# Performance work log

Measured on AMD Instinct MI355X. Metric: run time of the kernel, lower is better.

The kernel has to match this reference:

```python
import jax, jax.numpy as jnp
import numpy as np

TOPK = 8
EXTRA = 0  # ADDITIONAL_LAYERS_IN_GPU
CPU_TOPK = int(0.25 * 64)  # CPU_MOE_RATIO * num_experts = 16


def setup_inputs() -> dict:
    key = jax.random.key(0)
    k1, k2 = jax.random.split(key)
    hidden_states = jax.random.normal(k1, (4, 4096, 4096), dtype=jnp.float32)
    wg_weight = jax.random.normal(k2, (64, 4096), dtype=jnp.float32) * 0.02
    return {"hidden_states": hidden_states, "wg_weight": wg_weight}


def reference(hidden_states, wg_weight):
    bsz, seq_len, hidden_size = hidden_states.shape
    x = hidden_states.reshape(-1, hidden_size).astype(jnp.float32)  # [T, H]
    logits = jnp.einsum('th,eh->te', x, wg_weight)  # [T, 64]
    gates = jax.nn.softmax(logits, axis=1)
    values_all, indices_all = jax.lax.top_k(gates, TOPK + EXTRA)
    expert_weight = values_all[:, :TOPK]
    expert_index = indices_all[:, :TOPK]
    _, cpu_expert_index = jax.lax.top_k(gates, CPU_TOPK)
    cpu_expert_index = cpu_expert_index[:, 8 + EXTRA:]
    # norm_topk_prob=True, topk > 1
    eps = jnp.finfo(jnp.float32).eps
    denom = jnp.maximum(expert_weight.sum(axis=1, keepdims=True), eps)
    expert_weight = expert_weight / denom
    return (expert_weight, expert_index, cpu_expert_index, indices_all)
```

## Files before the change

### kernel.cpp

```cpp
#include <hip/hip_runtime.h>

#define T_TOK 16384
#define HDIM  4096
#define NEXP  64
#define TAU   2e-4f
#define BM    128

typedef unsigned short u16;
typedef u16   u16x8  __attribute__((ext_vector_type(8)));
typedef __bf16 bf16x8 __attribute__((ext_vector_type(8)));
typedef float f32x4  __attribute__((ext_vector_type(4)));

__global__ void zero_counter(int* counter) {
    if (threadIdx.x == 0) counter[0] = 0;
}

__global__ __launch_bounds__(256)
void wsplit_kernel(const float* __restrict__ w, u16x8* __restrict__ wfrag,
                   float4* __restrict__ wt4) {
    const int id  = blockIdx.x * 256 + threadIdx.x;
    const int e   = id >> 9;
    const int k8g = id & 511;
    const int k   = k8g * 8;

    const float* wp = w + (size_t)e * HDIM + k;
    const float4 v0 = *(const float4*)wp;
    const float4 v1 = *(const float4*)(wp + 4);

    wt4[(size_t)(2 * k8g) * NEXP + e]     = v0;
    wt4[(size_t)(2 * k8g + 1) * NEXP + e] = v1;

    const float fv[8] = {v0.x, v0.y, v0.z, v0.w, v1.x, v1.y, v1.z, v1.w};
    bf16x8 hv, lv;
#pragma unroll
    for (int j = 0; j < 8; ++j) {
        const __bf16 h = (__bf16)fv[j];
        hv[j] = h;
        lv[j] = (__bf16)(fv[j] - (float)h);
    }
    const int chunk = k >> 6;
    const int k8 = (k >> 3) & 7, ks = k8 >> 2, g = k8 & 3, nt = e >> 4;
    const int U = ks * 256 + nt * 64 + 16 * g + (e & 15);
    wfrag[(size_t)chunk * 1024 + U]       = __builtin_bit_cast(u16x8, hv);
    wfrag[(size_t)chunk * 1024 + 512 + U] = __builtin_bit_cast(u16x8, lv);
}

__global__ __launch_bounds__(256, 4)
void gate_gemm_mfma(const float* __restrict__ x, const u16x8* __restrict__ wfrag,
                    float* __restrict__ partial, int ksplit) {
    const int b      = blockIdx.x;
    const int kslice = b % ksplit;
    const int tblk   = b / ksplit;
    const int kspan  = HDIM / ksplit;
    const int k0     = kslice * kspan;
    const int t0     = tblk * BM;

    __shared__ __align__(16) u16 smem[2048 * 8];
    u16x8* smemv = (u16x8*)smem;

    const int tid  = threadIdx.x;
    const int lane = tid & 63;
    const int wv   = tid >> 6;

    f32x4 acc[2][4];
#pragma unroll
    for (int m = 0; m < 2; ++m)
#pragma unroll
        for (int nt = 0; nt < 4; ++nt) acc[m][nt] = (f32x4){0.f, 0.f, 0.f, 0.f};

    for (int kc = k0; kc < k0 + kspan; kc += 64) {
        __syncthreads();

#pragma unroll
        for (int i = 0; i < 4; ++i) {
            const int L   = tid + 256 * i;
            const int row = L >> 3;
            const int k8  = L & 7;
            const float* xp = x + (size_t)(t0 + row) * HDIM + kc + 8 * k8;
            const float4 v0 = *(const float4*)xp;
            const float4 v1 = *(const float4*)(xp + 4);
            const float fv[8] = {v0.x, v0.y, v0.z, v0.w, v1.x, v1.y, v1.z, v1.w};
            bf16x8 hv, lv;
#pragma unroll
            for (int j = 0; j < 8; ++j) {
                const __bf16 h = (__bf16)fv[j];
                hv[j] = h;
                lv[j] = (__bf16)(fv[j] - (float)h);
            }
            const int g = k8 & 3, ks = k8 >> 2, mt = row >> 4;
            const int U = ks * 512 + mt * 64 + 16 * g + (row & 15);
            const int phys = U ^ k8;
            smemv[phys]        = __builtin_bit_cast(u16x8, hv);
            smemv[1024 + phys] = __builtin_bit_cast(u16x8, lv);
        }
        __syncthreads();

        const u16x8* wsrc = wfrag + (size_t)(kc >> 6) * 1024;
#pragma unroll
        for (int ks2 = 0; ks2 < 2; ++ks2) {
            const int xo = (ks2 << 2) + (lane >> 4);
            bf16x8 axh[2], axl[2];
#pragma unroll
            for (int m = 0; m < 2; ++m) {
                const int ux = (ks2 * 512 + (wv * 2 + m) * 64 + lane) ^ xo;
                axh[m] = __builtin_bit_cast(bf16x8, smemv[ux]);
                axl[m] = __builtin_bit_cast(bf16x8, smemv[1024 + ux]);
            }
#pragma unroll
            for (int nt = 0; nt < 4; ++nt) {
                const int uwi = ks2 * 256 + nt * 64 + lane;
                const bf16x8 bh = __builtin_bit_cast(bf16x8, wsrc[uwi]);
                const bf16x8 bl = __builtin_bit_cast(bf16x8, wsrc[512 + uwi]);
#pragma unroll
                for (int m = 0; m < 2; ++m) {
                    acc[m][nt] = __builtin_amdgcn_mfma_f32_16x16x32_bf16(axh[m], bh, acc[m][nt], 0, 0, 0);
                    acc[m][nt] = __builtin_amdgcn_mfma_f32_16x16x32_bf16(axh[m], bl, acc[m][nt], 0, 0, 0);
                    acc[m][nt] = __builtin_amdgcn_mfma_f32_16x16x32_bf16(axl[m], bh, acc[m][nt], 0, 0, 0);
                }
            }
        }
    }

    float* op = partial + (size_t)kslice * T_TOK * NEXP;
    const int ecol = lane & 15;
#pragma unroll
    for (int m = 0; m < 2; ++m) {
        const int trow = t0 + (wv * 2 + m) * 16 + ((lane >> 4) << 2);
#pragma unroll
        for (int nt = 0; nt < 4; ++nt)
#pragma unroll
            for (int r = 0; r < 4; ++r)
                op[(size_t)(trow + r) * NEXP + nt * 16 + ecol] = acc[m][nt][r];
    }
}

__global__ __launch_bounds__(256)
void gate_topk_f32(const float* __restrict__ partial, int ksplit,
                   float* __restrict__ out, int* __restrict__ list,
                   int* __restrict__ counter) {
    const int wave = threadIdx.x >> 6;
    const int lane = threadIdx.x & 63;
    const int t = blockIdx.x * 4 + wave;

    float l = 0.f;
    for (int s = 0; s < ksplit; ++s)
        l += partial[(size_t)s * T_TOK * NEXP + (size_t)t * NEXP + lane];

    float v = l;
    const int idx = lane;
    float myval = -3.4e38f;
    int   myidx = 0;
#pragma unroll
    for (int r = 0; r < 17; ++r) {
        float bv = v;
        int   bi = idx;
#pragma unroll
        for (int s = 1; s < 64; s <<= 1) {
            const float ov = __shfl_xor(bv, s);
            const int   oi = __shfl_xor(bi, s);
            if (ov > bv || (ov == bv && oi < bi)) { bv = ov; bi = oi; }
        }
        if (lane == r) { myval = bv; myidx = bi; }
        if (idx == bi) v = -3.4e38f;
    }

    const float nxt = __shfl(myval, (lane + 1) & 63);
    const bool close = (lane < 16) && (myval - nxt < TAU);
    if (__ballot(close) != 0ull) {
        if (lane == 0) { const int p = atomicAdd(counter, 1); list[p] = t; }
    }

    const float m = __shfl(myval, 0);
    const float p = (lane < 16) ? expf(myval - m) : 0.f;
    float s8 = (lane < 8) ? p : 0.f;
#pragma unroll
    for (int s = 1; s < 64; s <<= 1) s8 += __shfl_xor(s8, s);

    float* ew = out;
    float* ei = out + (size_t)T_TOK * 8;
    float* ci = out + (size_t)2 * T_TOK * 8;
    float* ia = out + (size_t)3 * T_TOK * 8;
    if (lane < 8) {
        ew[(size_t)t * 8 + lane] = p / s8;
        ei[(size_t)t * 8 + lane] = (float)myidx;
        ia[(size_t)t * 8 + lane] = (float)myidx;
    } else if (lane < 16) {
        ci[(size_t)t * 8 + (lane - 8)] = (float)myidx;
    }
}

__global__ __launch_bounds__(256)
void repair_partial(const float* __restrict__ x, const float4* __restrict__ wt4,
                    const int* __restrict__ list, const int* __restrict__ counter,
                    double* __restrict__ fpart) {
    const int lane = threadIdx.x & 63;
    const int wid  = (int)((blockIdx.x * blockDim.x + threadIdx.x) >> 6);
    const int nw   = (int)((gridDim.x * blockDim.x) >> 6);
    const int nit  = counter[0] * 16;

    for (int it = wid; it < nit; it += nw) {
        const int li = it >> 4;
        const int ks = it & 15;
        const int t  = __builtin_amdgcn_readfirstlane(list[li]);
        const float4* xr4 = (const float4*)(x + (size_t)t * HDIM) + ks * 64;
        const float4* wb  = wt4 + (size_t)ks * 64 * NEXP;

        double a0 = 0.0, a1 = 0.0, a2 = 0.0, a3 = 0.0;
#pragma unroll 4
        for (int j = 0; j < 64; j += 4) {
            const float4 w0 = wb[(size_t)(j + 0) * NEXP + lane];
            const float4 w1 = wb[(size_t)(j + 1) * NEXP + lane];
            const float4 w2 = wb[(size_t)(j + 2) * NEXP + lane];
            const float4 w3 = wb[(size_t)(j + 3) * NEXP + lane];
            const float4 x0 = xr4[j + 0];
            const float4 x1 = xr4[j + 1];
            const float4 x2 = xr4[j + 2];
            const float4 x3 = xr4[j + 3];
            a0 = fma((double)x0.x, (double)w0.x, a0);
            a0 = fma((double)x0.y, (double)w0.y, a0);
            a0 = fma((double)x0.z, (double)w0.z, a0);
            a0 = fma((double)x0.w, (double)w0.w, a0);
            a1 = fma((double)x1.x, (double)w1.x, a1);
            a1 = fma((double)x1.y, (double)w1.y, a1);
            a1 = fma((double)x1.z, (double)w1.z, a1);
            a1 = fma((double)x1.w, (double)w1.w, a1);
            a2 = fma((double)x2.x, (double)w2.x, a2);
            a2 = fma((double)x2.y, (double)w2.y, a2);
            a2 = fma((double)x2.z, (double)w2.z, a2);
            a2 = fma((double)x2.w, (double)w2.w, a2);
            a3 = fma((double)x3.x, (double)w3.x, a3);
            a3 = fma((double)x3.y, (double)w3.y, a3);
            a3 = fma((double)x3.z, (double)w3.z, a3);
            a3 = fma((double)x3.w, (double)w3.w, a3);
        }
        fpart[(size_t)li * 1024 + ks * 64 + lane] = (a0 + a1) + (a2 + a3);
    }
}

__global__ __launch_bounds__(256)
void repair_final(const double* __restrict__ fpart, const int* __restrict__ list,
                  const int* __restrict__ counter, float* __restrict__ out) {
    const int lane = threadIdx.x & 63;
    const int wid  = (int)((blockIdx.x * blockDim.x + threadIdx.x) >> 6);
    const int nw   = (int)((gridDim.x * blockDim.x) >> 6);
    const int n    = counter[0];

    for (int li = wid; li < n; li += nw) {
        const int t = __builtin_amdgcn_readfirstlane(list[li]);

        double v = 0.0;
#pragma unroll
        for (int ks = 0; ks < 16; ++ks)
            v += fpart[(size_t)li * 1024 + ks * 64 + lane];

        const int idx = lane;
        double mylog = -1.0e308;
        int    myidx = 0;
#pragma unroll
        for (int r = 0; r < 16; ++r) {
            double bv = v;
            int    bi = idx;
#pragma unroll
            for (int s = 1; s < 64; s <<= 1) {
                const double ov = __shfl_xor(bv, s);
                const int    oi = __shfl_xor(bi, s);
                if (ov > bv || (ov == bv && oi < bi)) { bv = ov; bi = oi; }
            }
            if (lane == r) { mylog = bv; myidx = bi; }
            if (idx == bi) v = -1.0e308;
        }

        const double m = __shfl(mylog, 0);
        const float p = (lane < 16) ? expf((float)(mylog - m)) : 0.f;
        float s8 = (lane < 8) ? p : 0.f;
#pragma unroll
        for (int s = 1; s < 64; s <<= 1) s8 += __shfl_xor(s8, s);

        float* ew = out;
        float* ei = out + (size_t)T_TOK * 8;
        float* ci = out + (size_t)2 * T_TOK * 8;
        float* ia = out + (size_t)3 * T_TOK * 8;
        if (lane < 8) {
            ew[(size_t)t * 8 + lane] = p / s8;
            ei[(size_t)t * 8 + lane] = (float)myidx;
            ia[(size_t)t * 8 + lane] = (float)myidx;
        } else if (lane < 16) {
            ci[(size_t)t * 8 + (lane - 8)] = (float)myidx;
        }
    }
}

extern "C" void kernel_launch(void* const* d_in, const int* in_sizes, int n_in,
                              void* d_out, int out_size, void* d_ws, size_t ws_size,
                              hipStream_t stream) {
    const float* x = (const float*)d_in[0];
    const float* w = (const float*)d_in[1];
    float* out     = (float*)d_out;

    const size_t slice      = (size_t)T_TOK * NEXP * sizeof(float);
    const size_t wfragBytes = (size_t)64 * 1024 * 16;
    const size_t wt4Bytes   = (size_t)NEXP * HDIM * sizeof(float);
    const size_t fpartBytes = (size_t)T_TOK * 16 * NEXP * sizeof(double);
    const size_t extra      = wfragBytes + wt4Bytes + fpartBytes +
                              (size_t)T_TOK * sizeof(int) + 64;

    int ksplit = 1;
    if      (ws_size >= 4 * slice + extra) ksplit = 4;
    else if (ws_size >= 2 * slice + extra) ksplit = 2;

    float*  partial = (float*)d_ws;
    u16x8*  wfrag   = (u16x8*)((char*)d_ws + (size_t)ksplit * slice);
    float4* wt4     = (float4*)((char*)wfrag + wfragBytes);
    double* fpart   = (double*)((char*)wt4 + wt4Bytes);
    int*    list    = (int*)((char*)fpart + fpartBytes);
    int*    counter = list + T_TOK;

    zero_counter<<<1, 64, 0, stream>>>(counter);
    wsplit_kernel<<<128, 256, 0, stream>>>(w, wfrag, wt4);
    gate_gemm_mfma<<<ksplit * (T_TOK / BM), 256, 0, stream>>>(x, wfrag, partial, ksplit);
    gate_topk_f32<<<T_TOK / 4, 256, 0, stream>>>(partial, ksplit, out, list, counter);
    repair_partial<<<4096, 256, 0, stream>>>(x, wt4, list, counter, fpart);
    repair_final<<<1024, 256, 0, stream>>>(fpart, list, counter, out);
}
```

Measured before the change: 177.5 us.

## Load x and weight fragments via global_load_lds, convert to bf16 split at fragment read

The GEMM now stages raw fp32 x tiles and the pre-split weight fragments straight into LDS with direct global-to-LDS loads, using an XOR swizzle on the x tile. The bf16 hi/lo split of x moves from the staging store to the point where each wave reads its MFMA fragment. Weights are read from LDS instead of straight from global memory. It also permits an 8-way K split when the workspace is large enough and lowers the occupancy hint to 3 because of the larger 48KB LDS footprint. The goal is to cut register traffic and load latency in staging, at the cost of more LDS use and redundant conversion work.

```diff
diff --git a/kernel.cpp b/kernel.cpp
--- a/kernel.cpp
+++ b/kernel.cpp
@@ -10,6 +10,12 @@
 typedef u16   u16x8  __attribute__((ext_vector_type(8)));
 typedef __bf16 bf16x8 __attribute__((ext_vector_type(8)));
 typedef float f32x4  __attribute__((ext_vector_type(4)));
+
+__device__ __forceinline__ void gld16(const void* g, void* l) {
+    __builtin_amdgcn_global_load_lds(
+        (const __attribute__((address_space(1))) void*)g,
+        (__attribute__((address_space(3))) void*)l, 16, 0, 0);
+}
 
 __global__ void zero_counter(int* counter) {
     if (threadIdx.x == 0) counter[0] = 0;
@@ -45,7 +51,7 @@
     wfrag[(size_t)chunk * 1024 + 512 + U] = __builtin_bit_cast(u16x8, lv);
 }
 
-__global__ __launch_bounds__(256, 4)
+__global__ __launch_bounds__(256, 3)
 void gate_gemm_mfma(const float* __restrict__ x, const u16x8* __restrict__ wfrag,
                     float* __restrict__ partial, int ksplit) {
     const int b      = blockIdx.x;
@@ -55,8 +61,7 @@
     const int k0     = kslice * kspan;
     const int t0     = tblk * BM;
 
-    __shared__ __align__(16) u16 smem[2048 * 8];
-    u16x8* smemv = (u16x8*)smem;
+    __shared__ __align__(16) unsigned char smem[48 * 1024];
 
     const int tid  = threadIdx.x;
     const int lane = tid & 63;
@@ -71,46 +76,51 @@
     for (int kc = k0; kc < k0 + kspan; kc += 64) {
         __syncthreads();
 
+        const u16x8* wsrc = wfrag + (size_t)(kc >> 6) * 1024;
 #pragma unroll
         for (int i = 0; i < 4; ++i) {
-            const int L   = tid + 256 * i;
-            const int row = L >> 3;
-            const int k8  = L & 7;
-            const float* xp = x + (size_t)(t0 + row) * HDIM + kc + 8 * k8;
-            const float4 v0 = *(const float4*)xp;
-            const float4 v1 = *(const float4*)(xp + 4);
-            const float fv[8] = {v0.x, v0.y, v0.z, v0.w, v1.x, v1.y, v1.z, v1.w};
-            bf16x8 hv, lv;
-#pragma unroll
-            for (int j = 0; j < 8; ++j) {
-                const __bf16 h = (__bf16)fv[j];
-                hv[j] = h;
-                lv[j] = (__bf16)(fv[j] - (float)h);
-            }
-            const int g = k8 & 3, ks = k8 >> 2, mt = row >> 4;
-            const int U = ks * 512 + mt * 64 + 16 * g + (row & 15);
-            const int phys = U ^ k8;
-            smemv[phys]        = __builtin_bit_cast(u16x8, hv);
-            smemv[1024 + phys] = __builtin_bit_cast(u16x8, lv);
+            const int u = tid + 256 * i;
+            gld16(wsrc + u, smem + (size_t)u * 16);
+        }
+#pragma unroll
+        for (int j = 0; j < 8; ++j) {
+            const int u   = tid + 256 * j;
+            const int row = u >> 4;
+            const int k4l = (u & 15) ^ (row & 15);
+            gld16(x + (size_t)(t0 + row) * HDIM + kc + 4 * k4l,
+                  smem + 16384 + (size_t)u * 16);
         }
         __syncthreads();
 
-        const u16x8* wsrc = wfrag + (size_t)(kc >> 6) * 1024;
+        const u16*   wb = (const u16*)smem;
+        const float* xb = (const float*)(smem + 16384);
 #pragma unroll
         for (int ks2 = 0; ks2 < 2; ++ks2) {
-            const int xo = (ks2 << 2) + (lane >> 4);
+            const int k8 = (ks2 << 2) + (lane >> 4);
             bf16x8 axh[2], axl[2];
 #pragma unroll
             for (int m = 0; m < 2; ++m) {
-                const int ux = (ks2 * 512 + (wv * 2 + m) * 64 + lane) ^ xo;
-                axh[m] = __builtin_bit_cast(bf16x8, smemv[ux]);
-                axl[m] = __builtin_bit_cast(bf16x8, smemv[1024 + ux]);
+                const int row = (wv * 2 + m) * 16 + (lane & 15);
+                const int p0  = row * 16 + ((2 * k8) ^ (row & 15));
+                const int p1  = row * 16 + ((2 * k8 + 1) ^ (row & 15));
+                const float4 va = *(const float4*)(xb + 4 * p0);
+                const float4 vb = *(const float4*)(xb + 4 * p1);
+                const float fv[8] = {va.x, va.y, va.z, va.w, vb.x, vb.y, vb.z, vb.w};
+                bf16x8 hv, lv;
+#pragma unroll
+                for (int j = 0; j < 8; ++j) {
+                    const __bf16 h = (__bf16)fv[j];
+                    hv[j] = h;
+                    lv[j] = (__bf16)(fv[j] - (float)h);
+                }
+                axh[m] = hv;
+                axl[m] = lv;
             }
 #pragma unroll
             for (int nt = 0; nt < 4; ++nt) {
                 const int uwi = ks2 * 256 + nt * 64 + lane;
-                const bf16x8 bh = __builtin_bit_cast(bf16x8, wsrc[uwi]);
-                const bf16x8 bl = __builtin_bit_cast(bf16x8, wsrc[512 + uwi]);
+                const bf16x8 bh = __builtin_bit_cast(bf16x8, *(const u16x8*)(wb + (size_t)uwi * 8));
+                const bf16x8 bl = __builtin_bit_cast(bf16x8, *(const u16x8*)(wb + (size_t)(512 + uwi) * 8));
 #pragma unroll
                 for (int m = 0; m < 2; ++m) {
                     acc[m][nt] = __builtin_amdgcn_mfma_f32_16x16x32_bf16(axh[m], bh, acc[m][nt], 0, 0, 0);
@@ -305,7 +315,8 @@
                               (size_t)T_TOK * sizeof(int) + 64;
 
     int ksplit = 1;
-    if      (ws_size >= 4 * slice + extra) ksplit = 4;
+    if      (ws_size >= 8 * slice + extra) ksplit = 8;
+    else if (ws_size >= 4 * slice + extra) ksplit = 4;
     else if (ws_size >= 2 * slice + extra) ksplit = 2;
 
     float*  partial = (float*)d_ws;
```

New measurement: 159.5 us. -10.2%, faster.
